# Optimization experiments

Measured on AMD Instinct MI355X. Metric: run time of the kernel, lower is better.

Reference implementation:

```python
import jax, jax.numpy as jnp
import numpy as np

N_NODES = 100000
N_EDGES = 1600000
IN_F = 128
OUT_F = 32
HEADS = 4
NEG_SLOPE = 0.2
EPS = 1e-8


def setup_inputs() -> dict:
    key = jax.random.key(0)
    k1, k2, k3, k4 = jax.random.split(key, 4)
    x = jax.random.normal(k1, (N_NODES, IN_F), dtype=jnp.float32)
    # torch Linear weight layout: [out_features*num_heads, in_features]
    # xavier_uniform-like scale
    limW = float(np.sqrt(6.0 / (IN_F + OUT_F * HEADS)))
    W = jax.random.uniform(k2, (OUT_F * HEADS, IN_F), dtype=jnp.float32, minval=-limW, maxval=limW)
    lima = float(np.sqrt(6.0 / (HEADS + 2 * OUT_F)))
    a = jax.random.uniform(k3, (HEADS, 2 * OUT_F), dtype=jnp.float32, minval=-lima, maxval=lima)
    edge_index = jax.random.randint(k4, (2, N_EDGES), 0, N_NODES, dtype=jnp.int64)
    return {"x": x, "W": W, "a": a, "edge_index": edge_index}


def reference(x, W, a, edge_index):
    # x: [N, in], W: [H*F, in], a: [H, 2F], edge_index: [2, E]
    N = x.shape[0]
    H = HEADS
    F = OUT_F
    h = (x @ W.T).reshape(N, H, F)                      # [N, H, F]
    src, dst = edge_index[0], edge_index[1]
    h_src = h[src]                                       # [E, H, F]
    h_dst = h[dst]                                       # [E, H, F]
    # (cat([h_src, h_dst], -1) * a).sum(-1) == h_src@a_src + h_dst@a_dst
    a_src, a_dst = a[:, :F], a[:, F:]
    att = jnp.einsum('ehf,hf->eh', h_src, a_src) + jnp.einsum('ehf,hf->eh', h_dst, a_dst)  # [E, H]
    att = jnp.where(att >= 0, att, NEG_SLOPE * att)      # leaky_relu(0.2)
    att = jnp.exp(att - att.max())                       # global-max stabilization (as in source)
    att_sum = jax.ops.segment_sum(att, dst, num_segments=N)    # [N, H]
    att = att / (att_sum[dst] + EPS)                     # segment softmax
    # dropout is identity in eval mode
    out = jax.ops.segment_sum(att[..., None] * h_src, dst, num_segments=N)  # [N, H, F]
    return out.reshape(N, H * F)                         # concat=True
```

## Files before the change

kernel.cpp:

```cpp
#include <hip/hip_runtime.h>
#include <hip/hip_bf16.h>

#define NEG_SLOPE 0.2f
#define EPSV 1e-8f
#define BCAP 10240

typedef float f32x4 __attribute__((ext_vector_type(4)));
typedef short bf16x8 __attribute__((ext_vector_type(8)));
typedef unsigned short us8 __attribute__((ext_vector_type(8)));

static __device__ __forceinline__ float bf16tof(unsigned short s) {
    union { unsigned u; float f; } c; c.u = ((unsigned)s) << 16; return c.f;
}
static __device__ __forceinline__ unsigned short ftobf16(float f) {
    __hip_bfloat16 b = __float2bfloat16(f);
    return *(unsigned short*)&b;
}
static __device__ __forceinline__ float leaky_exp(float v) {
    v = fmaxf(v, NEG_SLOPE * v);
    return __expf(v);
}

__global__ __launch_bounds__(256, 2) void k_gemm(
        const float* __restrict__ x, const float* __restrict__ W,
        const float* __restrict__ a, unsigned short* __restrict__ h_bf,
        float* __restrict__ asrc, float* __restrict__ adst, int N) {
    __shared__ unsigned short xs[128 * 128];
    __shared__ unsigned short ws[128 * 128];
    __shared__ float sa[256];
    int tid = threadIdx.x;
    int nb = blockIdx.x * 128;

    sa[tid] = a[tid];

#pragma unroll
    for (int it = 0; it < 16; ++it) {
        int f = tid + 256 * it;
        int row = f >> 5;
        int k0 = (f & 31) << 2;
        int sw = row * 128 + (k0 ^ ((row & 7) << 3));
        int n = nb + row; if (n >= N) n = N - 1;
        float4 v = *(const float4*)(x + (size_t)n * 128 + k0);
        ushort4 o;
        o.x = ftobf16(v.x); o.y = ftobf16(v.y);
        o.z = ftobf16(v.z); o.w = ftobf16(v.w);
        *(ushort4*)&xs[sw] = o;
        float4 wv = *(const float4*)(W + (size_t)row * 128 + k0);
        ushort4 ow;
        ow.x = ftobf16(wv.x); ow.y = ftobf16(wv.y);
        ow.z = ftobf16(wv.z); ow.w = ftobf16(wv.w);
        *(ushort4*)&ws[sw] = ow;
    }
    __syncthreads();

    int w  = tid >> 6;
    int l  = tid & 63;
    int lr = l & 15;
    int lg = l >> 4;

    f32x4 acc[2][8];
    {
        f32x4 zz = {0.f, 0.f, 0.f, 0.f};
#pragma unroll
        for (int nt = 0; nt < 2; ++nt)
#pragma unroll
            for (int jt = 0; jt < 8; ++jt)
                acc[nt][jt] = zz;
    }

#pragma unroll
    for (int ks = 0; ks < 4; ++ks) {
        int kofs = ks * 32 + lg * 8;
        bf16x8 xf[2];
#pragma unroll
        for (int nt = 0; nt < 2; ++nt) {
            int row = w * 32 + nt * 16 + lr;
            xf[nt] = *(const bf16x8*)&xs[row * 128 + (kofs ^ ((row & 7) << 3))];
        }
#pragma unroll
        for (int jt = 0; jt < 8; ++jt) {
            int j = jt * 16 + lr;
            bf16x8 wf = *(const bf16x8*)&ws[j * 128 + (kofs ^ ((j & 7) << 3))];
#pragma unroll
            for (int nt = 0; nt < 2; ++nt)
                acc[nt][jt] = __builtin_amdgcn_mfma_f32_16x16x32_bf16(
                    wf, xf[nt], acc[nt][jt], 0, 0, 0);
        }
    }

#pragma unroll
    for (int g = 0; g < 4; ++g) {
        f32x4 as0 = *(const f32x4*)&sa[g * 64 +      lg * 4];
        f32x4 as1 = *(const f32x4*)&sa[g * 64 + 16 + lg * 4];
        f32x4 ad0 = *(const f32x4*)&sa[g * 64 + 32 + lg * 4];
        f32x4 ad1 = *(const f32x4*)&sa[g * 64 + 48 + lg * 4];
#pragma unroll
        for (int nt = 0; nt < 2; ++nt) {
            float ps = 0.f, pd = 0.f;
#pragma unroll
            for (int r = 0; r < 4; ++r) {
                ps += acc[nt][2 * g][r] * as0[r] + acc[nt][2 * g + 1][r] * as1[r];
                pd += acc[nt][2 * g][r] * ad0[r] + acc[nt][2 * g + 1][r] * ad1[r];
            }
            ps += __shfl_xor(ps, 16); pd += __shfl_xor(pd, 16);
            ps += __shfl_xor(ps, 32); pd += __shfl_xor(pd, 32);
            if (lg == 0) {
                int n = nb + w * 32 + nt * 16 + lr;
                if (n < N) {
                    asrc[(size_t)n * 4 + g] = ps;
                    adst[(size_t)n * 4 + g] = pd;
                }
            }
        }
    }

    __syncthreads();
#pragma unroll
    for (int nt = 0; nt < 2; ++nt) {
        int row = w * 32 + nt * 16 + lr;
        int m = (row & 7) << 3;
#pragma unroll
        for (int jt = 0; jt < 8; ++jt) {
            int j0 = jt * 16 + lg * 4;
            ushort4 o;
            o.x = ftobf16(acc[nt][jt][0]);
            o.y = ftobf16(acc[nt][jt][1]);
            o.z = ftobf16(acc[nt][jt][2]);
            o.w = ftobf16(acc[nt][jt][3]);
            *(ushort4*)&xs[row * 128 + (j0 ^ m)] = o;
        }
    }
    __syncthreads();
#pragma unroll
    for (int it = 0; it < 8; ++it) {
        int f = tid + 256 * it;
        int row = f >> 4;
        int c8 = (f & 15) << 3;
        int n = nb + row;
        if (n < N) {
            us8 v = *(const us8*)&xs[row * 128 + (c8 ^ ((row & 7) << 3))];
            *(us8*)(h_bf + (size_t)n * 128 + c8) = v;
        }
    }
}

__global__ __launch_bounds__(256) void k_bscatter(const int* __restrict__ ei,
        int* __restrict__ relcur, unsigned* __restrict__ ebuf, int E, int epb) {
    __shared__ int hist[256];
    __shared__ int wcur[256];
    __shared__ int bslot[256];
    int t = threadIdx.x;
    int lo = blockIdx.x * epb;
    int hi = min(E, lo + epb);
    hist[t] = 0;
    wcur[t] = 0;
    __syncthreads();
    int sreg[8], dreg[8];
    int cnt = 0;
#pragma unroll
    for (int k = 0; k < 8; k++) {
        int e = lo + t + 256 * k;
        if (e < hi) {
            sreg[k] = ei[e];
            dreg[k] = ei[E + e];
            atomicAdd(&hist[dreg[k] >> 9], 1);
            cnt = k + 1;
        }
    }
    __syncthreads();
    int c = hist[t];
    int res = c ? atomicAdd(&relcur[t], c) : 0;
    bslot[t] = t * BCAP + res;
    __syncthreads();
    for (int k = 0; k < cnt; k++) {
        int s = sreg[k];
        int d = dreg[k];
        int b = d >> 9;
        int off = atomicAdd(&wcur[b], 1);
        int slot = bslot[b] + off;
        if (slot < (b + 1) * BCAP)
            ebuf[slot] = ((unsigned)(d & 511) << 23) | (unsigned)s;
    }
}

__global__ __launch_bounds__(256) void k_bscan(const int* __restrict__ relcur,
                                               int* __restrict__ gbase,
                                               int* __restrict__ row_ptr,
                                               int NBK, int N, int E) {
    __shared__ int sm[256];
    int t = threadIdx.x;
    int c = (t < NBK) ? min(relcur[t], BCAP) : 0;
    sm[t] = c;
    __syncthreads();
    for (int off = 1; off < 256; off <<= 1) {
        int u = (t >= off) ? sm[t - off] : 0;
        __syncthreads();
        sm[t] += u;
        __syncthreads();
    }
    gbase[t] = sm[t] - c;
    if (t == 0) row_ptr[N] = E;
}

__global__ __launch_bounds__(256) void k_build(const int* __restrict__ relcur,
        const int* __restrict__ gbase, const unsigned* __restrict__ ebuf,
        int* __restrict__ row_ptr, int* __restrict__ csr_src, int N) {
    __shared__ int hist[512];
    __shared__ int excl[512];
    __shared__ int sm[256];
    int b = blockIdx.x;
    int t = threadIdx.x;
    int cnt = min(relcur[b], BCAP);
    int base = gbase[b];
    int d0 = b << 9;
    const unsigned* ep = ebuf + (size_t)b * BCAP;

    hist[t] = 0; hist[t + 256] = 0;
    __syncthreads();
    for (int i = t; i < cnt; i += 256)
        atomicAdd(&hist[ep[i] >> 23], 1);
    __syncthreads();

    int a0 = hist[2 * t], a1 = hist[2 * t + 1];
    int s = a0 + a1;
    sm[t] = s;
    __syncthreads();
    for (int off = 1; off < 256; off <<= 1) {
        int u = (t >= off) ? sm[t - off] : 0;
        __syncthreads();
        sm[t] += u;
        __syncthreads();
    }
    int ex = sm[t] - s;
    excl[2 * t] = ex;
    excl[2 * t + 1] = ex + a0;
    int n0 = d0 + 2 * t, n1 = d0 + 2 * t + 1;
    if (n0 < N) row_ptr[n0] = base + ex;
    if (n1 < N) row_ptr[n1] = base + ex + a0;
    __syncthreads();

    for (int i = t; i < cnt; i += 256) {
        unsigned p = ep[i];
        int pos = base + atomicAdd(&excl[p >> 23], 1);
        csr_src[pos] = (int)(p & 0x7FFFFFu);
    }
}

__global__ __launch_bounds__(256) void k_agg(
        const int* __restrict__ row_ptr, const int* __restrict__ csr_src,
        const float* __restrict__ asrc, const float* __restrict__ adst,
        const unsigned short* __restrict__ h_bf,
        float* __restrict__ out, int N) {
    __shared__ int   se[4][2][68];
    __shared__ float sw[4][2][272];
    int tid = threadIdx.x;
    int w  = tid >> 6;
    int l  = tid & 63;
    int gg = l >> 4;
    int m  = l & 15;
    int hh = m >> 2;

    int n = blockIdx.x * 16 + w * 4 + gg;
    bool valid = (n < N);
    int nc = valid ? n : (N - 1);
    int lo  = row_ptr[nc];
    int deg = row_ptr[nc + 1] - lo;
    float4 dv = *(const float4*)(adst + 4 * (size_t)nc);

    int md = deg;
    md = max(md, __shfl_xor(md, 16));
    md = max(md, __shfl_xor(md, 32));
    int nch = (md + 15) >> 4;

    float acc[8] = {};
    float asum = 0.f;
    const unsigned short* hp = h_bf + 8 * m;

#define ACC8(U, WT) do { \
        union { unsigned u; float f; } q; \
        q.u = (U).x << 16;         acc[0] += (WT) * q.f; \
        q.u = (U).x & 0xFFFF0000u; acc[1] += (WT) * q.f; \
        q.u = (U).y << 16;         acc[2] += (WT) * q.f; \
        q.u = (U).y & 0xFFFF0000u; acc[3] += (WT) * q.f; \
        q.u = (U).z << 16;         acc[4] += (WT) * q.f; \
        q.u = (U).z & 0xFFFF0000u; acc[5] += (WT) * q.f; \
        q.u = (U).w << 16;         acc[6] += (WT) * q.f; \
        q.u = (U).w & 0xFFFF0000u; acc[7] += (WT) * q.f; \
    } while (0)

    if (m < deg) {
        int s = csr_src[lo + m];
        se[w][0][17 * gg + m] = s;
        float4 sv = *(const float4*)(asrc + 4 * (size_t)s);
        float4 wv;
        wv.x = leaky_exp(sv.x + dv.x);
        wv.y = leaky_exp(sv.y + dv.y);
        wv.z = leaky_exp(sv.z + dv.z);
        wv.w = leaky_exp(sv.w + dv.w);
        *(float4*)&sw[w][0][68 * gg + 4 * m] = wv;
    }

    for (int c = 0; c < nch; ++c) {
        int cb = c & 1;
        int sN = 0; float4 svN; bool haveN = false;
        {
            int eN = (c + 1) * 16 + m;
            if (c + 1 < nch && eN < deg) {
                sN = csr_src[lo + eN];
                svN = *(const float4*)(asrc + 4 * (size_t)sN);
                haveN = true;
            }
        }
        __builtin_amdgcn_wave_barrier();
        int base16 = c * 16;
        int cnt = min(deg - base16, 16);
        const int*   sep = &se[w][cb][17 * gg];
        const float* swp = &sw[w][cb][68 * gg];
        int i = 0;
        uint4 u0, u1;
        if (cnt >= 2) {
            u0 = *(const uint4*)(hp + (size_t)sep[0] * 128);
            u1 = *(const uint4*)(hp + (size_t)sep[1] * 128);
        }
        for (; i + 4 <= cnt; i += 2) {
            uint4 t0 = *(const uint4*)(hp + (size_t)sep[i + 2] * 128);
            uint4 t1 = *(const uint4*)(hp + (size_t)sep[i + 3] * 128);
            float w0 = swp[4 * i + hh];
            float w1 = swp[4 * i + 4 + hh];
            ACC8(u0, w0);
            ACC8(u1, w1);
            asum += w0 + w1;
            u0 = t0; u1 = t1;
        }
        if (i + 2 <= cnt) {
            float w0 = swp[4 * i + hh];
            float w1 = swp[4 * i + 4 + hh];
            ACC8(u0, w0);
            ACC8(u1, w1);
            asum += w0 + w1;
            i += 2;
        }
        for (; i < cnt; ++i) {
            int s0 = sep[i];
            float w0 = swp[4 * i + hh];
            uint4 uu = *(const uint4*)(hp + (size_t)s0 * 128);
            ACC8(uu, w0);
            asum += w0;
        }
        if (haveN) {
            se[w][cb ^ 1][17 * gg + m] = sN;
            float4 wv;
            wv.x = leaky_exp(svN.x + dv.x);
            wv.y = leaky_exp(svN.y + dv.y);
            wv.z = leaky_exp(svN.z + dv.z);
            wv.w = leaky_exp(svN.w + dv.w);
            *(float4*)&sw[w][cb ^ 1][68 * gg + 4 * m] = wv;
        }
        __builtin_amdgcn_wave_barrier();
    }
#undef ACC8

    if (valid) {
        float inv = 1.f / (asum + EPSV);
        float4 o0, o1;
        o0.x = acc[0] * inv; o0.y = acc[1] * inv;
        o0.z = acc[2] * inv; o0.w = acc[3] * inv;
        o1.x = acc[4] * inv; o1.y = acc[5] * inv;
        o1.z = acc[6] * inv; o1.w = acc[7] * inv;
        *(float4*)(out + (size_t)n * 128 + 8 * m) = o0;
        *(float4*)(out + (size_t)n * 128 + 8 * m + 4) = o1;
    }
}

extern "C" void kernel_launch(void* const* d_in, const int* in_sizes, int n_in,
                              void* d_out, int out_size, void* d_ws, size_t ws_size,
                              hipStream_t stream) {
    const float* x = (const float*)d_in[0];
    const float* W = (const float*)d_in[1];
    const float* a = (const float*)d_in[2];
    const int* ei = (const int*)d_in[3];
    float* out = (float*)d_out;

    int N = in_sizes[0] / 128;
    int E = in_sizes[3] / 2;
    int NBK = (N + 511) >> 9;

    char* wsb = (char*)d_ws;
    size_t off = 0;
    auto alloc = [&](size_t bytes) -> void* {
        void* p = wsb + off;
        off += (bytes + 255) / 256 * 256;
        return p;
    };
    unsigned short* h_bf = (unsigned short*)alloc((size_t)N * 128 * 2);
    float* asrc = (float*)alloc((size_t)N * 4 * 4);
    float* adst = (float*)alloc((size_t)N * 4 * 4);
    int* row_ptr = (int*)alloc((size_t)(N + 1) * 4);
    int* relcur = (int*)alloc(256 * 4);
    int* gbase = (int*)alloc(256 * 4);
    unsigned* ebuf = (unsigned*)alloc((size_t)NBK * BCAP * 4);
    int* csr_src = (int*)alloc((size_t)E * 4);

    hipMemsetAsync(relcur, 0, 256 * 4, stream);

    dim3 ggrid((N + 127) / 128);
    k_gemm<<<ggrid, 256, 0, stream>>>(x, W, a, h_bf, asrc, adst, N);
    int nsb = (E + 2047) / 2048;
    k_bscatter<<<nsb, 256, 0, stream>>>(ei, relcur, ebuf, E, 2048);
    k_bscan<<<1, 256, 0, stream>>>(relcur, gbase, row_ptr, NBK, N, E);
    k_build<<<NBK, 256, 0, stream>>>(relcur, gbase, ebuf, row_ptr, csr_src, N);
    k_agg<<<(N + 15) / 16, 256, 0, stream>>>(row_ptr, csr_src, asrc, adst, h_bf, out, N);
}
```

Before: 235.6 us.

## Halve CSR bucket width and fold bucket scan into build kernel

Result: faster. 225.1 us (-4.5%).

```diff
diff --git a/kernel.cpp b/kernel.cpp
--- a/kernel.cpp
+++ b/kernel.cpp
@@ -3,7 +3,7 @@
 
 #define NEG_SLOPE 0.2f
 #define EPSV 1e-8f
-#define BCAP 10240
+#define BCAP 5632
 
 typedef float f32x4 __attribute__((ext_vector_type(4)));
 typedef short bf16x8 __attribute__((ext_vector_type(8)));
@@ -144,26 +144,26 @@
     }
 }
 
-__global__ __launch_bounds__(256) void k_bscatter(const int* __restrict__ ei,
+__global__ __launch_bounds__(512) void k_bscatter(const int* __restrict__ ei,
         int* __restrict__ relcur, unsigned* __restrict__ ebuf, int E, int epb) {
-    __shared__ int hist[256];
-    __shared__ int wcur[256];
-    __shared__ int bslot[256];
+    __shared__ int hist[512];
+    __shared__ int wcur[512];
+    __shared__ int bslot[512];
     int t = threadIdx.x;
     int lo = blockIdx.x * epb;
     int hi = min(E, lo + epb);
     hist[t] = 0;
     wcur[t] = 0;
     __syncthreads();
-    int sreg[8], dreg[8];
+    int sreg[4], dreg[4];
     int cnt = 0;
 #pragma unroll
-    for (int k = 0; k < 8; k++) {
-        int e = lo + t + 256 * k;
+    for (int k = 0; k < 4; k++) {
+        int e = lo + t + 512 * k;
         if (e < hi) {
             sreg[k] = ei[e];
             dreg[k] = ei[E + e];
-            atomicAdd(&hist[dreg[k] >> 9], 1);
+            atomicAdd(&hist[dreg[k] >> 8], 1);
             cnt = k + 1;
         }
     }
@@ -175,71 +175,64 @@
     for (int k = 0; k < cnt; k++) {
         int s = sreg[k];
         int d = dreg[k];
-        int b = d >> 9;
+        int b = d >> 8;
         int off = atomicAdd(&wcur[b], 1);
         int slot = bslot[b] + off;
         if (slot < (b + 1) * BCAP)
-            ebuf[slot] = ((unsigned)(d & 511) << 23) | (unsigned)s;
-    }
-}
-
-__global__ __launch_bounds__(256) void k_bscan(const int* __restrict__ relcur,
-                                               int* __restrict__ gbase,
-                                               int* __restrict__ row_ptr,
-                                               int NBK, int N, int E) {
-    __shared__ int sm[256];
-    int t = threadIdx.x;
-    int c = (t < NBK) ? min(relcur[t], BCAP) : 0;
-    sm[t] = c;
-    __syncthreads();
-    for (int off = 1; off < 256; off <<= 1) {
-        int u = (t >= off) ? sm[t - off] : 0;
-        __syncthreads();
-        sm[t] += u;
-        __syncthreads();
-    }
-    gbase[t] = sm[t] - c;
-    if (t == 0) row_ptr[N] = E;
-}
-
-__global__ __launch_bounds__(256) void k_build(const int* __restrict__ relcur,
-        const int* __restrict__ gbase, const unsigned* __restrict__ ebuf,
-        int* __restrict__ row_ptr, int* __restrict__ csr_src, int N) {
-    __shared__ int hist[512];
-    __shared__ int excl[512];
-    __shared__ int sm[256];
+            ebuf[slot] = ((unsigned)(d & 255) << 23) | (unsigned)s;
+    }
+}
+
+__global__ __launch_bounds__(512) void k_build(const int* __restrict__ relcur,
+        const unsigned* __restrict__ ebuf,
+        int* __restrict__ row_ptr, int* __restrict__ csr_src,
+        int NBK, int N, int E) {
+    __shared__ int smA[512];
+    __shared__ int hist[256];
+    __shared__ int smB[256];
+    __shared__ int excl[256];
     int b = blockIdx.x;
     int t = threadIdx.x;
-    int cnt = min(relcur[b], BCAP);
-    int base = gbase[b];
-    int d0 = b << 9;
+
+    smA[t] = (t < NBK) ? min(relcur[t], BCAP) : 0;
+    __syncthreads();
+    for (int off = 1; off < 512; off <<= 1) {
+        int u = (t >= off) ? smA[t - off] : 0;
+        __syncthreads();
+        smA[t] += u;
+        __syncthreads();
+    }
+    int cnt  = min(relcur[b], BCAP);
+    int base = smA[b] - cnt;
+    if (b == 0 && t == 0) row_ptr[N] = E;
+
+    int d0 = b << 8;
     const unsigned* ep = ebuf + (size_t)b * BCAP;
 
-    hist[t] = 0; hist[t + 256] = 0;
-    __syncthreads();
-    for (int i = t; i < cnt; i += 256)
+    if (t < 256) hist[t] = 0;
+    __syncthreads();
+    for (int i = t; i < cnt; i += 512)
         atomicAdd(&hist[ep[i] >> 23], 1);
     __syncthreads();
 
-    int a0 = hist[2 * t], a1 = hist[2 * t + 1];
-    int s = a0 + a1;
-    sm[t] = s;
+    int s = (t < 256) ? hist[t] : 0;
+    if (t < 256) smB[t] = s;
     __syncthreads();
     for (int off = 1; off < 256; off <<= 1) {
-        int u = (t >= off) ? sm[t - off] : 0;
+        int u = (t >= off && t < 256) ? smB[t - off] : 0;
         __syncthreads();
-        sm[t] += u;
+        if (t < 256) smB[t] += u;
         __syncthreads();
     }
-    int ex = sm[t] - s;
-    excl[2 * t] = ex;
-    excl[2 * t + 1] = ex + a0;
-    int n0 = d0 + 2 * t, n1 = d0 + 2 * t + 1;
-    if (n0 < N) row_ptr[n0] = base + ex;
-    if (n1 < N) row_ptr[n1] = base + ex + a0;
-    __syncthreads();
-
-    for (int i = t; i < cnt; i += 256) {
+    if (t < 256) {
+        int ex = smB[t] - s;
+        excl[t] = ex;
+        int node = d0 + t;
+        if (node < N) row_ptr[node] = base + ex;
+    }
+    __syncthreads();
+
+    for (int i = t; i < cnt; i += 512) {
         unsigned p = ep[i];
         int pos = base + atomicAdd(&excl[p >> 23], 1);
         csr_src[pos] = (int)(p & 0x7FFFFFu);
@@ -383,7 +376,7 @@
 
     int N = in_sizes[0] / 128;
     int E = in_sizes[3] / 2;
-    int NBK = (N + 511) >> 9;
+    int NBK = (N + 255) >> 8;
 
     char* wsb = (char*)d_ws;
     size_t off = 0;
@@ -396,18 +389,16 @@
     float* asrc = (float*)alloc((size_t)N * 4 * 4);
     float* adst = (float*)alloc((size_t)N * 4 * 4);
     int* row_ptr = (int*)alloc((size_t)(N + 1) * 4);
-    int* relcur = (int*)alloc(256 * 4);
-    int* gbase = (int*)alloc(256 * 4);
+    int* relcur = (int*)alloc(512 * 4);
     unsigned* ebuf = (unsigned*)alloc((size_t)NBK * BCAP * 4);
     int* csr_src = (int*)alloc((size_t)E * 4);
 
-    hipMemsetAsync(relcur, 0, 256 * 4, stream);
+    hipMemsetAsync(relcur, 0, 512 * 4, stream);
 
     dim3 ggrid((N + 127) / 128);
     k_gemm<<<ggrid, 256, 0, stream>>>(x, W, a, h_bf, asrc, adst, N);
     int nsb = (E + 2047) / 2048;
-    k_bscatter<<<nsb, 256, 0, stream>>>(ei, relcur, ebuf, E, 2048);
-    k_bscan<<<1, 256, 0, stream>>>(relcur, gbase, row_ptr, NBK, N, E);
-    k_build<<<NBK, 256, 0, stream>>>(relcur, gbase, ebuf, row_ptr, csr_src, N);
+    k_bscatter<<<nsb, 512, 0, stream>>>(ei, relcur, ebuf, E, 2048);
+    k_build<<<NBK, 512, 0, stream>>>(relcur, ebuf, row_ptr, csr_src, NBK, N, E);
     k_agg<<<(N + 15) / 16, 256, 0, stream>>>(row_ptr, csr_src, asrc, adst, h_bf, out, N);
 }
```
